# Kernel optimization log

Measured on AMD Instinct MI355X. Metric: run time of the kernel, lower is better.

Reference implementation:

```python
import jax, jax.numpy as jnp
import numpy as np

N_NODES = 15279  # hardcoded in the original forward's reshape


def spmm(rows, cols, vals, dense):
    # sparse [N,N] @ dense [N,F] via gather + segment-sum over COO edges
    gathered = dense[cols] * vals[:, None]          # [E, F]
    return jax.ops.segment_sum(gathered, rows, num_segments=N_NODES)


def setup_inputs() -> dict:
    key = jax.random.key(0)
    ks = jax.random.split(key, 10)
    E = 488928  # 15279 nodes * avg_degree 32
    emb_num, emb_dim = 10000, 128
    in_ch, n_hid, n_class = 1024, 512, 16

    x = jax.random.randint(ks[0], (N_NODES, 8), 0, emb_num, dtype=jnp.int64)
    adj_rows = jax.random.randint(ks[1], (E,), 0, N_NODES, dtype=jnp.int32)
    adj_cols = jax.random.randint(ks[2], (E,), 0, N_NODES, dtype=jnp.int32)
    adj_vals = jax.random.uniform(ks[3], (E,), dtype=jnp.float32)

    emb_table = jax.random.normal(ks[4], (emb_num + 1, emb_dim), dtype=jnp.float32) * 0.02
    emb_table = emb_table.at[0].set(0.0)  # padding_idx=0

    # Kipf GraphConvolution init: uniform(-1/sqrt(fan_out), 1/sqrt(fan_out))
    s1 = 1.0 / np.sqrt(n_hid)
    W1 = jax.random.uniform(ks[5], (in_ch, n_hid), minval=-s1, maxval=s1, dtype=jnp.float32)
    b1 = jax.random.uniform(ks[6], (n_hid,), minval=-s1, maxval=s1, dtype=jnp.float32)
    s2 = 1.0 / np.sqrt(n_class)
    W2 = jax.random.uniform(ks[7], (n_hid, n_class), minval=-s2, maxval=s2, dtype=jnp.float32)
    b2 = jax.random.uniform(ks[8], (n_class,), minval=-s2, maxval=s2, dtype=jnp.float32)

    return {"x": x, "adj_rows": adj_rows, "adj_cols": adj_cols, "adj_vals": adj_vals,
            "emb_table": emb_table, "W1": W1, "b1": b1, "W2": W2, "b2": b2}


def reference(x, adj_rows, adj_cols, adj_vals, emb_table, W1, b1, W2, b2):
    # embedding lookup + relu, flatten to [15279, in_ch]
    h = jax.nn.relu(emb_table[x])                  # [N, 8, emb_dim]
    h = h.reshape(N_NODES, -1)                     # [N, in_ch]
    # gc1: adj @ (h @ W1) + b1, then relu (dropout is identity in eval)
    h = jax.nn.relu(spmm(adj_rows, adj_cols, adj_vals, h @ W1) + b1)
    # gc2: adj @ (h @ W2) + b2
    return spmm(adj_rows, adj_cols, adj_vals, h @ W2) + b2
```

## Files before the change

### kernel.cpp

```cpp
#include <hip/hip_runtime.h>

#define NNODES 15279
#define NEDGE  488928
#define INCH   1024
#define NHID   512
#define NCLS   16
#define EMBROWS 10001
#define BCAP   128

#define NB_EMBR 1251
#define NB_W1T  128
#define NB_SCAT 1910
#define NB_GEMM1 960

using short8 = __attribute__((ext_vector_type(8))) short;
using f32x4  = __attribute__((ext_vector_type(4))) float;
using f32x2  = __attribute__((ext_vector_type(2))) float;

__device__ __forceinline__ float asf(unsigned int u) {
  union { unsigned int i; float f; } v; v.i = u; return v.f;
}
__device__ __forceinline__ unsigned short f2bf(float f) {
  union { float ff; unsigned int i; } v; v.ff = f;
  return (unsigned short)((v.i + 0x7FFFu + ((v.i >> 16) & 1u)) >> 16);
}

__global__ __launch_bounds__(256) void k_prep_scatter(
    const float* __restrict__ emb, unsigned short* __restrict__ embr,
    const float* __restrict__ W1, unsigned short* __restrict__ w1t,
    const int* __restrict__ rows, const int* __restrict__ cols,
    const float* __restrict__ vals,
    int* __restrict__ cursor, unsigned int* __restrict__ bpack) {
  __shared__ float tile[64][65];
  int b = blockIdx.x;
  int t = threadIdx.x;
  if (b < NB_EMBR) {
    int g = b * 256 + t;
    if (g * 4 < EMBROWS * 128) {
      const float4 v = *(const float4*)&emb[g * 4];
      unsigned int lo = (unsigned int)f2bf(fmaxf(v.x, 0.f)) | ((unsigned int)f2bf(fmaxf(v.y, 0.f)) << 16);
      unsigned int hi = (unsigned int)f2bf(fmaxf(v.z, 0.f)) | ((unsigned int)f2bf(fmaxf(v.w, 0.f)) << 16);
      uint2 o; o.x = lo; o.y = hi;
      *(uint2*)&embr[g * 4] = o;
    }
  } else if (b < NB_EMBR + NB_W1T) {
    int b2 = b - NB_EMBR;
    int k0 = (b2 & 15) * 64, n0 = (b2 >> 4) * 64;
    int c = t & 63, r4 = t >> 6;
    for (int i = 0; i < 16; ++i) {
      int r = r4 + i * 4;
      tile[r][c] = W1[(k0 + r) * NHID + n0 + c];
    }
    __syncthreads();
    for (int i = 0; i < 16; ++i) {
      int nr = r4 + i * 4;
      w1t[(size_t)(n0 + nr) * INCH + k0 + c] = f2bf(tile[c][nr]);
    }
  } else {
    int e = (b - NB_EMBR - NB_W1T) * 256 + t;
    if (e < NEDGE) {
      int r = rows[e];
      int idx = atomicAdd(&cursor[r], 1);
      if (idx < BCAP) {
        bpack[r * BCAP + idx] = ((unsigned int)cols[e] << 16) | (unsigned int)f2bf(vals[e]);
      }
    }
  }
}

__global__ __launch_bounds__(256) void k_gemm1(const int* __restrict__ x,
                                               const unsigned short* __restrict__ embr,
                                               const unsigned short* __restrict__ Bt,
                                               unsigned short* __restrict__ Cs) {
  __shared__ unsigned short As[128 * 64];
  __shared__ unsigned short Bs[64 * 64];
  const int t = threadIdx.x;
  const int m0 = (blockIdx.x >> 3) * 128;
  const int n0 = (blockIdx.x & 7) * 64;
  const int w = t >> 6, l = t & 63;
  const int wm = w >> 1, wn = w & 1;
  const int l4 = l >> 4, l15 = l & 15;
  const int rowA = wm * 64 + l15;
  const int colB = wn * 32 + l15;
  f32x4 acc[4][2] = {};

  int xidx[4][8];
#pragma unroll
  for (int i = 0; i < 4; ++i) {
    int grow = m0 + (t >> 3) + i * 32;
    grow = grow < NNODES ? grow : NNODES - 1;
    *(int4*)&xidx[i][0] = *(const int4*)&x[grow * 8];
    *(int4*)&xidx[i][4] = *(const int4*)&x[grow * 8 + 4];
  }

#pragma unroll
  for (int kt = 0; kt < 16; ++kt) {
    const int k0 = kt * 64;
    const int s = kt >> 1;
    const int dbase = (kt & 1) * 64;
#pragma unroll
    for (int i = 0; i < 4; ++i) {
      int p = i * 256 + t;
      int row = i * 32 + (t >> 3);
      int skg = ((t & 7) ^ (row & 7)) * 8;
      __builtin_amdgcn_global_load_lds(
          (const __attribute__((address_space(1))) void*)&embr[(size_t)xidx[i][s] * 128 + dbase + skg],
          (__attribute__((address_space(3))) void*)&As[p * 8], 16, 0, 0);
    }
#pragma unroll
    for (int i = 0; i < 2; ++i) {
      int p = i * 256 + t;
      int row = i * 32 + (t >> 3);
      int skg = ((t & 7) ^ (row & 7)) * 8;
      __builtin_amdgcn_global_load_lds(
          (const __attribute__((address_space(1))) void*)&Bt[(size_t)(n0 + row) * INCH + k0 + skg],
          (__attribute__((address_space(3))) void*)&Bs[p * 8], 16, 0, 0);
    }
    __syncthreads();
#pragma unroll
    for (int kk = 0; kk < 2; ++kk) {
      short8 af[4], bfr[2];
#pragma unroll
      for (int m = 0; m < 4; ++m) {
        int r = rowA + m * 16;
        af[m] = *(const short8*)&As[(r * 8 + ((kk * 4 + l4) ^ (r & 7))) * 8];
      }
#pragma unroll
      for (int n = 0; n < 2; ++n) {
        int c = colB + n * 16;
        bfr[n] = *(const short8*)&Bs[(c * 8 + ((kk * 4 + l4) ^ (c & 7))) * 8];
      }
#pragma unroll
      for (int m = 0; m < 4; ++m)
#pragma unroll
        for (int n = 0; n < 2; ++n)
          acc[m][n] = __builtin_amdgcn_mfma_f32_16x16x32_bf16(af[m], bfr[n], acc[m][n], 0, 0, 0);
    }
    __syncthreads();
  }
  const int rb = m0 + wm * 64 + l4 * 4;
  const int cb = wn * 32 + l15;
  unsigned short* Cb = Cs + (size_t)(n0 >> 6) * NNODES * 64;
#pragma unroll
  for (int m = 0; m < 4; ++m)
#pragma unroll
    for (int j = 0; j < 4; ++j) {
      int r = rb + m * 16 + j;
      if (r < NNODES) {
        Cb[(size_t)r * 64 + cb]      = f2bf(acc[m][0][j]);
        Cb[(size_t)r * 64 + cb + 16] = f2bf(acc[m][1][j]);
      }
    }
}

__global__ __launch_bounds__(256) void k_spmm1(const int* __restrict__ cnt,
                                               const unsigned int* __restrict__ bpack,
                                               const unsigned short* __restrict__ t1s,
                                               const float* __restrict__ b1,
                                               unsigned short* __restrict__ h1) {
  int b = blockIdx.x;
  int slice = b & 7;
  int rgrp = b >> 3;
  int t = threadIdx.x;
  int wid = t >> 6, lane = t & 63;
  int rloc = lane >> 4, el = (lane >> 3) & 1, ft = lane & 7;
  int r = rgrp * 16 + wid * 4 + rloc;
  bool valid = r < NNODES;
  int rr = valid ? r : NNODES - 1;
  const char* tbase = (const char*)(t1s + (size_t)slice * NNODES * 64) + ft * 16;
  int fglob = slice * 64 + ft * 8;
  int e0 = rr * BCAP;
  int c0n = cnt[rr]; c0n = c0n < BCAP ? c0n : BCAP;
  int e1 = valid ? e0 + c0n : e0;
  f32x2 acc[4] = {};
  int e = e0 + el;
  for (; e + 2 < e1; e += 4) {
    unsigned int uA = bpack[e], uB = bpack[e + 2];
    uint4 a  = *(const uint4*)(tbase + ((size_t)(uA >> 16) << 7));
    uint4 bq = *(const uint4*)(tbase + ((size_t)(uB >> 16) << 7));
    float vA = asf(uA << 16), vB = asf(uB << 16);
    f32x2 vA2 = {vA, vA}, vB2 = {vB, vB};
    unsigned int ua[4] = {a.x, a.y, a.z, a.w};
    unsigned int ub[4] = {bq.x, bq.y, bq.z, bq.w};
#pragma unroll
    for (int d = 0; d < 4; ++d) {
      f32x2 pa = {asf(ua[d] << 16), asf(ua[d] & 0xffff0000u)};
      f32x2 pb = {asf(ub[d] << 16), asf(ub[d] & 0xffff0000u)};
      acc[d] += vA2 * pa;
      acc[d] += vB2 * pb;
    }
  }
  for (; e < e1; e += 2) {
    unsigned int u = bpack[e];
    uint4 a = *(const uint4*)(tbase + ((size_t)(u >> 16) << 7));
    float v = asf(u << 16);
    f32x2 v2 = {v, v};
    unsigned int ua[4] = {a.x, a.y, a.z, a.w};
#pragma unroll
    for (int d = 0; d < 4; ++d) {
      f32x2 p = {asf(ua[d] << 16), asf(ua[d] & 0xffff0000u)};
      acc[d] += v2 * p;
    }
  }
#pragma unroll
  for (int d = 0; d < 4; ++d) {
    acc[d].x += __shfl_xor(acc[d].x, 8);
    acc[d].y += __shfl_xor(acc[d].y, 8);
  }
  if (el == 0 && valid) {
    unsigned int o[4];
#pragma unroll
    for (int d = 0; d < 4; ++d) {
      float s0 = fmaxf(acc[d].x + b1[fglob + 2 * d], 0.f);
      float s1 = fmaxf(acc[d].y + b1[fglob + 2 * d + 1], 0.f);
      o[d] = (unsigned int)f2bf(s0) | ((unsigned int)f2bf(s1) << 16);
    }
    uint4 ov; ov.x = o[0]; ov.y = o[1]; ov.z = o[2]; ov.w = o[3];
    *(uint4*)&h1[(size_t)r * NHID + fglob] = ov;
  }
}

__global__ __launch_bounds__(256) void k_gemm2(const unsigned short* __restrict__ h1,
                                               const float* __restrict__ W2,
                                               float* __restrict__ t2) {
  __shared__ unsigned short w2t[16 * 520];
  int t = threadIdx.x;
#pragma unroll
  for (int i = 0; i < 32; ++i) {
    int p = i * 256 + t;
    int k = p >> 4, f = p & 15;
    w2t[f * 520 + k] = f2bf(W2[p]);
  }
  int w = t >> 6, l = t & 63;
  int l15 = l & 15, l4 = l >> 4;
  int r0 = blockIdx.x * 64 + w * 16;
  int row = r0 + l15; row = row < NNODES ? row : NNODES - 1;
  short8 af[16];
#pragma unroll
  for (int kk = 0; kk < 16; ++kk)
    af[kk] = *(const short8*)&h1[(size_t)row * NHID + kk * 32 + l4 * 8];
  __syncthreads();
  f32x4 acc = {};
#pragma unroll
  for (int kk = 0; kk < 16; ++kk) {
    short8 bfr = *(const short8*)&w2t[l15 * 520 + kk * 32 + l4 * 8];
    acc = __builtin_amdgcn_mfma_f32_16x16x32_bf16(af[kk], bfr, acc, 0, 0, 0);
  }
#pragma unroll
  for (int j = 0; j < 4; ++j) {
    int r = r0 + l4 * 4 + j;
    if (r < NNODES) t2[(size_t)r * NCLS + l15] = acc[j];
  }
}

__global__ __launch_bounds__(256) void k_spmm2(const int* __restrict__ cnt,
                                               const unsigned int* __restrict__ bpack,
                                               const float* __restrict__ t2,
                                               const float* __restrict__ b2,
                                               float* __restrict__ out) {
  int t = threadIdx.x;
  int f = t & 15, rl = t >> 4;
  int r = blockIdx.x * 16 + rl;
  if (r >= NNODES) return;
  const char* t2b = (const char*)t2 + f * 4;
  int e0 = r * BCAP;
  int n = cnt[r]; n = n < BCAP ? n : BCAP;
  int e1 = e0 + n;
  float a0 = 0.f, a1 = 0.f, a2 = 0.f, a3 = 0.f;
  int e = e0;
  for (; e + 3 < e1; e += 4) {
    unsigned int u0 = bpack[e], u1 = bpack[e + 1], u2 = bpack[e + 2], u3 = bpack[e + 3];
    a0 += asf(u0 << 16) * *(const float*)(t2b + ((size_t)(u0 >> 16) << 6));
    a1 += asf(u1 << 16) * *(const float*)(t2b + ((size_t)(u1 >> 16) << 6));
    a2 += asf(u2 << 16) * *(const float*)(t2b + ((size_t)(u2 >> 16) << 6));
    a3 += asf(u3 << 16) * *(const float*)(t2b + ((size_t)(u3 >> 16) << 6));
  }
  for (; e < e1; ++e) {
    unsigned int u = bpack[e];
    a0 += asf(u << 16) * *(const float*)(t2b + ((size_t)(u >> 16) << 6));
  }
  out[(size_t)r * NCLS + f] = (a0 + a1) + (a2 + a3) + b2[f];
}

extern "C" void kernel_launch(void* const* d_in, const int* in_sizes, int n_in,
                              void* d_out, int out_size, void* d_ws, size_t ws_size,
                              hipStream_t stream) {
  (void)in_sizes; (void)n_in; (void)out_size; (void)ws_size;
  const int*   x    = (const int*)  d_in[0];
  const int*   rows = (const int*)  d_in[1];
  const int*   cols = (const int*)  d_in[2];
  const float* vals = (const float*)d_in[3];
  const float* emb  = (const float*)d_in[4];
  const float* W1   = (const float*)d_in[5];
  const float* b1   = (const float*)d_in[6];
  const float* W2   = (const float*)d_in[7];
  const float* b2   = (const float*)d_in[8];
  float* out = (float*)d_out;

  char* ws = (char*)d_ws;
  size_t off = 0;
  auto take = [&](size_t bytes) {
    char* p = ws + off;
    off = (off + bytes + 255) & ~(size_t)255;
    return p;
  };
  unsigned short* embr = (unsigned short*)take((size_t)EMBROWS * 128 * 2);
  unsigned short* w1t  = (unsigned short*)take((size_t)NHID * INCH * 2);
  unsigned short* t1s  = (unsigned short*)take((size_t)NNODES * NHID * 2);
  unsigned short* h1   = (unsigned short*)take((size_t)NNODES * NHID * 2);
  float*          t2   = (float*)take((size_t)NNODES * NCLS * 4);
  int*            cursor = (int*)take((size_t)NNODES * 4);
  unsigned int*   bpack  = (unsigned int*)take((size_t)NNODES * BCAP * 4);

  hipMemsetAsync(cursor, 0, (size_t)NNODES * 4, stream);

  k_prep_scatter<<<NB_EMBR + NB_W1T + NB_SCAT, 256, 0, stream>>>(
      emb, embr, W1, w1t, rows, cols, vals, cursor, bpack);
  k_gemm1<<<NB_GEMM1, 256, 0, stream>>>(x, embr, w1t, t1s);
  k_spmm1<<<((NNODES + 15) / 16) * 8, 256, 0, stream>>>(cursor, bpack, t1s, b1, h1);
  k_gemm2<<<(NNODES + 63) / 64, 256, 0, stream>>>(h1, W2, t2);
  k_spmm2<<<(NNODES + 15) / 16, 256, 0, stream>>>(cursor, bpack, t2, b2, out);
}
```

Before: 111.3 us.

## Overlap edge bucketing with GEMM1 and pipeline SpMM1 gathers four-wide

Moves the COO edge bucketing (atomic scatter into per-row slots) out of the prep kernel and into extra blocks of the GEMM1 launch, so the latency-bound scatter runs alongside the compute-bound GEMM instead of before it. The SpMM1 inner loop now processes four edges per step and prefetches the next four packed edge words while gathering the current ones, to raise memory-level parallelism. The cost is higher register pressure in SpMM1, and scatter blocks now reserve the GEMM's shared memory, which can lower their occupancy.

Result: faster. 97.02 us (-12.9%).

```diff
diff --git a/kernel.cpp b/kernel.cpp
--- a/kernel.cpp
+++ b/kernel.cpp
@@ -10,8 +10,8 @@
 
 #define NB_EMBR 1251
 #define NB_W1T  128
+#define NB_GEMM1 960
 #define NB_SCAT 1910
-#define NB_GEMM1 960
 
 using short8 = __attribute__((ext_vector_type(8))) short;
 using f32x4  = __attribute__((ext_vector_type(4))) float;
@@ -25,12 +25,10 @@
   return (unsigned short)((v.i + 0x7FFFu + ((v.i >> 16) & 1u)) >> 16);
 }
 
-__global__ __launch_bounds__(256) void k_prep_scatter(
-    const float* __restrict__ emb, unsigned short* __restrict__ embr,
-    const float* __restrict__ W1, unsigned short* __restrict__ w1t,
-    const int* __restrict__ rows, const int* __restrict__ cols,
-    const float* __restrict__ vals,
-    int* __restrict__ cursor, unsigned int* __restrict__ bpack) {
+__global__ __launch_bounds__(256) void k_prep(const float* __restrict__ emb,
+                                              unsigned short* __restrict__ embr,
+                                              const float* __restrict__ W1,
+                                              unsigned short* __restrict__ w1t) {
   __shared__ float tile[64][65];
   int b = blockIdx.x;
   int t = threadIdx.x;
@@ -43,7 +41,7 @@
       uint2 o; o.x = lo; o.y = hi;
       *(uint2*)&embr[g * 4] = o;
     }
-  } else if (b < NB_EMBR + NB_W1T) {
+  } else {
     int b2 = b - NB_EMBR;
     int k0 = (b2 & 15) * 64, n0 = (b2 >> 4) * 64;
     int c = t & 63, r4 = t >> 6;
@@ -56,8 +54,24 @@
       int nr = r4 + i * 4;
       w1t[(size_t)(n0 + nr) * INCH + k0 + c] = f2bf(tile[c][nr]);
     }
-  } else {
-    int e = (b - NB_EMBR - NB_W1T) * 256 + t;
+  }
+}
+
+__global__ __launch_bounds__(256) void k_gemm1_scatter(
+    const int* __restrict__ x,
+    const unsigned short* __restrict__ embr,
+    const unsigned short* __restrict__ Bt,
+    unsigned short* __restrict__ Cs,
+    const int* __restrict__ rows,
+    const int* __restrict__ cols,
+    const float* __restrict__ vals,
+    int* __restrict__ cursor,
+    unsigned int* __restrict__ bpack) {
+  __shared__ unsigned short As[128 * 64];
+  __shared__ unsigned short Bs[64 * 64];
+  const int t = threadIdx.x;
+  if (blockIdx.x >= NB_GEMM1) {
+    int e = (blockIdx.x - NB_GEMM1) * 256 + t;
     if (e < NEDGE) {
       int r = rows[e];
       int idx = atomicAdd(&cursor[r], 1);
@@ -65,16 +79,8 @@
         bpack[r * BCAP + idx] = ((unsigned int)cols[e] << 16) | (unsigned int)f2bf(vals[e]);
       }
     }
-  }
-}
-
-__global__ __launch_bounds__(256) void k_gemm1(const int* __restrict__ x,
-                                               const unsigned short* __restrict__ embr,
-                                               const unsigned short* __restrict__ Bt,
-                                               unsigned short* __restrict__ Cs) {
-  __shared__ unsigned short As[128 * 64];
-  __shared__ unsigned short Bs[64 * 64];
-  const int t = threadIdx.x;
+    return;
+  }
   const int m0 = (blockIdx.x >> 3) * 128;
   const int n0 = (blockIdx.x & 7) * 64;
   const int w = t >> 6, l = t & 63;
@@ -173,35 +179,58 @@
   int c0n = cnt[rr]; c0n = c0n < BCAP ? c0n : BCAP;
   int e1 = valid ? e0 + c0n : e0;
   f32x2 acc[4] = {};
-  int e = e0 + el;
-  for (; e + 2 < e1; e += 4) {
-    unsigned int uA = bpack[e], uB = bpack[e + 2];
-    uint4 a  = *(const uint4*)(tbase + ((size_t)(uA >> 16) << 7));
-    uint4 bq = *(const uint4*)(tbase + ((size_t)(uB >> 16) << 7));
-    float vA = asf(uA << 16), vB = asf(uB << 16);
-    f32x2 vA2 = {vA, vA}, vB2 = {vB, vB};
-    unsigned int ua[4] = {a.x, a.y, a.z, a.w};
-    unsigned int ub[4] = {bq.x, bq.y, bq.z, bq.w};
-#pragma unroll
-    for (int d = 0; d < 4; ++d) {
-      f32x2 pa = {asf(ua[d] << 16), asf(ua[d] & 0xffff0000u)};
-      f32x2 pb = {asf(ub[d] << 16), asf(ub[d] & 0xffff0000u)};
-      acc[d] += vA2 * pa;
-      acc[d] += vB2 * pb;
-    }
-  }
-  for (; e < e1; e += 2) {
-    unsigned int u = bpack[e];
+  int p = e0 + el;
+
+#define GFMA4(U0, U1, U2, U3) do {                                          \
+    uint4 g0 = *(const uint4*)(tbase + ((size_t)((U0) >> 16) << 7));        \
+    uint4 g1 = *(const uint4*)(tbase + ((size_t)((U1) >> 16) << 7));        \
+    uint4 g2 = *(const uint4*)(tbase + ((size_t)((U2) >> 16) << 7));        \
+    uint4 g3 = *(const uint4*)(tbase + ((size_t)((U3) >> 16) << 7));        \
+    float v0 = asf((U0) << 16), v1 = asf((U1) << 16);                       \
+    float v2 = asf((U2) << 16), v3 = asf((U3) << 16);                       \
+    f32x2 w0 = {v0, v0}, w1 = {v1, v1}, w2 = {v2, v2}, w3 = {v3, v3};       \
+    unsigned int a0[4] = {g0.x, g0.y, g0.z, g0.w};                          \
+    unsigned int a1[4] = {g1.x, g1.y, g1.z, g1.w};                          \
+    unsigned int a2[4] = {g2.x, g2.y, g2.z, g2.w};                          \
+    unsigned int a3[4] = {g3.x, g3.y, g3.z, g3.w};                          \
+    _Pragma("unroll")                                                       \
+    for (int d = 0; d < 4; ++d) {                                           \
+      f32x2 p0 = {asf(a0[d] << 16), asf(a0[d] & 0xffff0000u)};              \
+      f32x2 p1 = {asf(a1[d] << 16), asf(a1[d] & 0xffff0000u)};              \
+      f32x2 p2 = {asf(a2[d] << 16), asf(a2[d] & 0xffff0000u)};              \
+      f32x2 p3 = {asf(a3[d] << 16), asf(a3[d] & 0xffff0000u)};              \
+      acc[d] += w0 * p0;                                                    \
+      acc[d] += w1 * p1;                                                    \
+      acc[d] += w2 * p2;                                                    \
+      acc[d] += w3 * p3;                                                    \
+    }                                                                       \
+  } while (0)
+
+  if (p + 6 < e1) {
+    unsigned int u0 = bpack[p], u1 = bpack[p + 2], u2 = bpack[p + 4], u3 = bpack[p + 6];
+    int q = p + 8;
+    for (; q + 6 < e1; q += 8) {
+      unsigned int n0 = bpack[q],     n1 = bpack[q + 2];
+      unsigned int n2 = bpack[q + 4], n3 = bpack[q + 6];
+      GFMA4(u0, u1, u2, u3);
+      u0 = n0; u1 = n1; u2 = n2; u3 = n3;
+    }
+    GFMA4(u0, u1, u2, u3);
+    p = q;
+  }
+  for (; p < e1; p += 2) {
+    unsigned int u = bpack[p];
     uint4 a = *(const uint4*)(tbase + ((size_t)(u >> 16) << 7));
     float v = asf(u << 16);
     f32x2 v2 = {v, v};
     unsigned int ua[4] = {a.x, a.y, a.z, a.w};
 #pragma unroll
     for (int d = 0; d < 4; ++d) {
-      f32x2 p = {asf(ua[d] << 16), asf(ua[d] & 0xffff0000u)};
-      acc[d] += v2 * p;
-    }
-  }
+      f32x2 pp = {asf(ua[d] << 16), asf(ua[d] & 0xffff0000u)};
+      acc[d] += v2 * pp;
+    }
+  }
+#undef GFMA4
 #pragma unroll
   for (int d = 0; d < 4; ++d) {
     acc[d].x += __shfl_xor(acc[d].x, 8);
@@ -314,9 +343,9 @@
 
   hipMemsetAsync(cursor, 0, (size_t)NNODES * 4, stream);
 
-  k_prep_scatter<<<NB_EMBR + NB_W1T + NB_SCAT, 256, 0, stream>>>(
-      emb, embr, W1, w1t, rows, cols, vals, cursor, bpack);
-  k_gemm1<<<NB_GEMM1, 256, 0, stream>>>(x, embr, w1t, t1s);
+  k_prep<<<NB_EMBR + NB_W1T, 256, 0, stream>>>(emb, embr, W1, w1t);
+  k_gemm1_scatter<<<NB_GEMM1 + NB_SCAT, 256, 0, stream>>>(
+      x, embr, w1t, t1s, rows, cols, vals, cursor, bpack);
   k_spmm1<<<((NNODES + 15) / 16) * 8, 256, 0, stream>>>(cursor, bpack, t1s, b1, h1);
   k_gemm2<<<(NNODES + 63) / 64, 256, 0, stream>>>(h1, W2, t2);
   k_spmm2<<<(NNODES + 15) / 16, 256, 0, stream>>>(cursor, bpack, t2, b2, out);
```
